# Performance work log

Measured on AMD Instinct MI355X. Metric: run time of the kernel, lower is better.

The kernel has to match this reference:

```python
import jax, jax.numpy as jnp
import numpy as np
from jax import lax

L = 25            # max_delay (250 // init_spike_step=10, odd)
SIG = 12.0        # max_delay // 2, frozen (requires_grad=False)
BN_EPS = 1e-5
EPS = 1e-7


def _dcls_kernel(W, P):
    # Gaussian interpolation of kernel_count=1 weights onto a dense kernel of size L.
    # W, P: (out, in). Returns (out, in, L).
    grid = jnp.arange(L, dtype=W.dtype) - L // 2          # (L,)
    K = jnp.exp(-0.5 * ((grid[None, None, :] - P[:, :, None]) / SIG) ** 2)
    K = K / (jnp.sum(K, axis=-1, keepdims=True) + EPS)    # normalize over kernel taps
    return W[:, :, None] * K


def _dcls_conv(x_tbc, W, P):
    # x_tbc: (T, B, Cin) -> causal dilated-kernel conv over time -> (T, B, Cout)
    kernel = _dcls_kernel(W, P)                           # (Cout, Cin, L)
    xb = jnp.transpose(x_tbc, (1, 2, 0))                  # (B, Cin, T)
    xb = jnp.pad(xb, ((0, 0), (0, 0), (L - 1, 0)))        # left (causal) padding
    y = lax.conv_general_dilated(xb, kernel, window_strides=(1,), padding='VALID',
                                 dimension_numbers=('NCH', 'OIH', 'NCH'))
    return jnp.transpose(y, (2, 0, 1))                    # (T, B, Cout)


def _bn(x_tbc, gamma, beta):
    # BatchNorm1d with step_mode='m': stats over merged (T, B) per channel.
    mean = jnp.mean(x_tbc, axis=(0, 1))
    var = jnp.var(x_tbc, axis=(0, 1))
    xhat = (x_tbc - mean) * lax.rsqrt(var + BN_EPS)
    return gamma * xhat + beta


def setup_inputs() -> dict:
    key = jax.random.key(0)
    ks = jax.random.split(key, 8)
    B, T, C = 128, 100, 700
    x = jax.random.uniform(ks[0], (B, T, C), dtype=jnp.float32)
    pmax = float(L // 2)
    W1 = jax.random.normal(ks[1], (256, 700), jnp.float32) * (1.0 / np.sqrt(700))
    P1 = jax.random.uniform(ks[2], (256, 700), jnp.float32, minval=-pmax, maxval=pmax)
    W2 = jax.random.normal(ks[3], (256, 256), jnp.float32) * (1.0 / np.sqrt(256))
    P2 = jax.random.uniform(ks[4], (256, 256), jnp.float32, minval=-pmax, maxval=pmax)
    W3 = jax.random.normal(ks[5], (20, 256), jnp.float32) * (1.0 / np.sqrt(256))
    P3 = jax.random.uniform(ks[6], (20, 256), jnp.float32, minval=-pmax, maxval=pmax)
    return {
        'x': x, 'W1': W1, 'P1': P1, 'W2': W2, 'P2': P2, 'W3': W3, 'P3': P3,
        'gamma1': jnp.ones((256,), jnp.float32), 'beta1': jnp.zeros((256,), jnp.float32),
        'gamma2': jnp.ones((256,), jnp.float32), 'beta2': jnp.zeros((256,), jnp.float32),
    }


def reference(x, W1, P1, W2, P2, W3, P3, gamma1, beta1, gamma2, beta2):
    h = jnp.transpose(x, (1, 0, 2))            # (T, B, C)
    h = _dcls_conv(h, W1, P1)                  # (T, B, 256)
    h = jax.nn.relu(_bn(h, gamma1, beta1))     # dropout = identity (eval)
    h = _dcls_conv(h, W2, P2)                  # (T, B, 256)
    h = jax.nn.relu(_bn(h, gamma2, beta2))
    h = _dcls_conv(h, W3, P3)                  # (T, B, 20)
    return jnp.sum(jax.nn.softmax(h, axis=2), axis=0)   # (B, 20)
```

## Files before the change

### kernel.cpp

```cpp
#include <hip/hip_runtime.h>
#include <stdint.h>


#define T_LEN 100
#define B_SZ  128
#define M_ROWS 12800
#define R_RANK 4
#define K_FIR 448

typedef __bf16 v8bf __attribute__((ext_vector_type(8)));
typedef float  v4f  __attribute__((ext_vector_type(4)));
typedef unsigned int uint32;
typedef unsigned short ushort_t;

struct PhiT { float v[25][R_RANK]; };
constexpr double cexp_(double x) {
  double s = 1.0, t = 1.0;
  for (int n = 1; n < 30; ++n) { t = t * x / n; s += t; }
  return s;
}
constexpr PhiT make_phi() {
  PhiT P{};
  for (int tau = 0; tau < 25; ++tau) {
    double u = (tau - 12) / 12.0;
    double g = cexp_(-0.5 * u * u);
    double T0 = 1.0, T1 = u;
    P.v[tau][0] = (float)(g * T0);
    P.v[tau][1] = (float)(g * T1);
    for (int r = 2; r < R_RANK; ++r) {
      double T2 = 2.0 * u * T1 - T0;
      P.v[tau][r] = (float)(g * T2);
      T0 = T1; T1 = T2;
    }
  }
  return P;
}
constexpr PhiT PHI = make_phi();

__device__ __forceinline__ void gl_lds16(const void* g, void* l) {
  __builtin_amdgcn_global_load_lds(
      (const __attribute__((address_space(1))) char*)g,
      (__attribute__((address_space(3))) char*)l, 16, 0, 0);
}

__device__ __forceinline__ void build_wr_body(
    const float* __restrict__ W, const float* __restrict__ P,
    __bf16* __restrict__ Wr, int CIN, int CINP, int COUT, int COUTP, int o) {
  for (int i = threadIdx.x; i < CINP; i += blockDim.x) {
    bool valid = (o < COUT) && (i < CIN);
    float w = valid ? W[(size_t)o * CIN + i] : 0.f;
    float p = valid ? P[(size_t)o * CIN + i] : 0.f;
    float S = 0.f;
#pragma unroll
    for (int l = 0; l < 25; ++l) {
      float d = ((float)(l - 12) - p) * (1.f / 12.f);
      S += expf(-0.5f * d * d);
    }
    float v = p * (1.f / 12.f);
    float g = w * expf(-0.5f * v * v) / (S + 1e-7f);
    float h = 0.5f * v, hh = h * h;
    float pw = 1.f;
#pragma unroll
    for (int r = 0; r < R_RANK; ++r) {
      float term = pw, sum = pw;
#pragma unroll
      for (int m = 1; m <= 6; ++m) {
        term *= hh / (float)(m * (m + r));
        sum += term;
      }
      float c = g * ((r == 0) ? 1.f : 2.f) * sum;
      Wr[((size_t)r * COUTP + o) * CINP + i] = (__bf16)c;
      pw *= h / (float)(r + 1);
    }
  }
}

__global__ void setup_all(const float* __restrict__ x,
                          const float* __restrict__ W1, const float* __restrict__ P1,
                          const float* __restrict__ W2, const float* __restrict__ P2,
                          const float* __restrict__ W3, const float* __restrict__ P3,
                          __bf16* __restrict__ Xb, __bf16* __restrict__ Wr1,
                          __bf16* __restrict__ Wr2, __bf16* __restrict__ Wr3,
                          __bf16* __restrict__ Af, float* __restrict__ stats) {
  int blk = blockIdx.x;
  if (blk < 256) { build_wr_body(W1, P1, Wr1, 700, 704, 256, 256, blk); return; }
  blk -= 256;
  if (blk < 256) { build_wr_body(W2, P2, Wr2, 256, 256, 256, 256, blk); return; }
  blk -= 256;
  if (blk < 32) { build_wr_body(W3, P3, Wr3, 256, 256, 20, 32, blk); return; }
  blk -= 32;
  if (blk < 196) {
    int idx = blk * 256 + threadIdx.x;
    if (idx < 112 * 448) {
      int t = idx / 448, k = idx - t * 448;
      float v = 0.f;
      if (t < 100 && k < 400) {
        int r = k / 100, s = k - r * 100;
        int tau = s - t + 24;
        if (tau >= 0 && tau < 25) v = PHI.v[tau][r];
      }
      Af[idx] = (__bf16)v;
    }
    return;
  }
  blk -= 196;
  if (blk < 12800) {
    int t = blk >> 7, b = blk & 127;
    const float* src = x + ((size_t)b * T_LEN + t) * 700;
    __bf16* dst = Xb + (size_t)blk * 704;
    for (int c = threadIdx.x; c < 704; c += 256) dst[c] = (c < 700) ? (__bf16)src[c] : (__bf16)0.f;
    return;
  }
  blk -= 12800;
  if (blk == 0) {
    for (int i = threadIdx.x; i < 1024; i += 256) stats[i] = 0.f;
  }
}

template <int CINP, int BLK_N, int WROWS, int WCOLS, int CO_SH, bool BN>
__global__ __launch_bounds__(256, 2)
void gemm_rk64(const __bf16* __restrict__ A, const __bf16* __restrict__ Bm,
               __bf16* __restrict__ Z,
               const float* __restrict__ stats, const float* __restrict__ gamma,
               const float* __restrict__ beta) {
  constexpr int COUTP = 1 << CO_SH;
  constexpr int WM = 128 / WROWS;
  constexpr int WN = BLK_N / WCOLS;
  constexpr int RM = WM / 16;
  constexpr int RN = WN / 16;
  __shared__ __align__(16) __bf16 sA[128 * 64];
  __shared__ __align__(16) __bf16 sB[BLK_N * 64];
  __shared__ float sScale[BN ? 256 : 1];
  __shared__ float sShift[BN ? 256 : 1];

  const int tid = threadIdx.x;
  const int w = tid >> 6, lane = tid & 63;
  const int q = lane >> 4, ln = lane & 15;
  const int wrow = w / WCOLS, wcol = w % WCOLS;
  const int srow8 = lane >> 3;
  const int s8 = lane & 7;
  const int g_lane = s8 ^ srow8;

  const int t0 = blockIdx.x;
  const int oc = blockIdx.y * BLK_N;
  const __bf16* Abase = A + (size_t)t0 * 128 * CINP;
  const __bf16* Bbase = Bm + (size_t)oc * CINP;

  if (BN) {
    int c = tid;
    float mean = stats[c] * (1.f / 12800.f);
    float var = stats[256 + c] * (1.f / 12800.f) - mean * mean;
    float sc = rsqrtf(var + 1e-5f) * gamma[c];
    sScale[c] = sc;
    sShift[c] = beta[c] - mean * sc;
    __syncthreads();
  }

  v4f acc[RM][RN];
#pragma unroll
  for (int a = 0; a < RM; ++a)
#pragma unroll
    for (int b = 0; b < RN; ++b) acc[a][b] = v4f{0.f, 0.f, 0.f, 0.f};

  for (int ic = 0; ic < CINP; ic += 64) {
    if (!BN) {
      for (int j = w; j < 16; j += 4) {
        int m = j * 8 + srow8;
        int g = s8 ^ (m & 7);
        gl_lds16(Abase + (size_t)m * CINP + ic + g * 8, &sA[j * 512]);
      }
    } else {
      float scl[8], sht[8];
#pragma unroll
      for (int jj = 0; jj < 8; ++jj) {
        scl[jj] = sScale[ic + g_lane * 8 + jj];
        sht[jj] = sShift[ic + g_lane * 8 + jj];
      }
      for (int j = w; j < 16; j += 4) {
        int m = j * 8 + srow8;
        uint4 raw = *(const uint4*)(Abase + (size_t)m * CINP + ic + g_lane * 8);
        const ushort_t* pr = (const ushort_t*)&raw;
        uint4 outv;
        ushort_t* po = (ushort_t*)&outv;
#pragma unroll
        for (int jj = 0; jj < 8; ++jj) {
          uint32 u = (uint32)pr[jj] << 16;
          float yv; __builtin_memcpy(&yv, &u, 4);
          float vv = fmaxf(yv * scl[jj] + sht[jj], 0.f);
          __bf16 bv = (__bf16)vv;
          po[jj] = *(const ushort_t*)&bv;
        }
        *(uint4*)((char*)sA + (size_t)j * 1024 + (size_t)lane * 16) = outv;
      }
    }
    for (int j = w; j < BLK_N / 8; j += 4) {
      int n = j * 8 + srow8;
      int g = s8 ^ (n & 7);
      gl_lds16(Bbase + (size_t)n * CINP + ic + g * 8, &sB[j * 512]);
    }
    __syncthreads();

#pragma unroll
    for (int s = 0; s < 2; ++s) {
      v8bf af[RM], bfr[RN];
#pragma unroll
      for (int a = 0; a < RM; ++a) {
        int m = wrow * WM + a * 16 + ln;
        af[a] = *(const v8bf*)&sA[m * 64 + ((((s << 2) | q) ^ (m & 7)) * 8)];
      }
#pragma unroll
      for (int b = 0; b < RN; ++b) {
        int n = wcol * WN + b * 16 + ln;
        bfr[b] = *(const v8bf*)&sB[n * 64 + ((((s << 2) | q) ^ (n & 7)) * 8)];
      }
#pragma unroll
      for (int a = 0; a < RM; ++a)
#pragma unroll
        for (int b = 0; b < RN; ++b)
          acc[a][b] = __builtin_amdgcn_mfma_f32_16x16x32_bf16(af[a], bfr[b], acc[a][b], 0, 0, 0);
    }
    __syncthreads();
  }

#pragma unroll
  for (int a = 0; a < RM; ++a) {
#pragma unroll
    for (int b = 0; b < RN; ++b) {
      int n = oc + wcol * WN + b * 16 + ln;
      int r = n >> CO_SH, o = n & (COUTP - 1);
#pragma unroll
      for (int rr = 0; rr < 4; ++rr) {
        int m = t0 * 128 + wrow * WM + a * 16 + q * 4 + rr;
        Z[((size_t)r * M_ROWS + m) * COUTP + o] = (__bf16)acc[a][b][rr];
      }
    }
  }
}

template <int COUTP, bool STATS, bool SOFTMAX>
__global__ __launch_bounds__(256, 2)
void fir_gemm64(const __bf16* __restrict__ Af, const __bf16* __restrict__ Z,
                __bf16* __restrict__ Yout, float* __restrict__ stats,
                float* __restrict__ outp, int N) {
  __shared__ __align__(16) unsigned char smem[26624];
  __bf16* sA = (__bf16*)smem;
  uint32* sBu = (uint32*)(smem + 14336);

  const int tid = threadIdx.x;
  const int w = tid >> 6, lane = tid & 63;
  const int q = lane >> 4, ln = lane & 15;
  const int srow8 = lane >> 3, s8 = lane & 7;
  const int kp = tid >> 3;
  const int noct = tid & 7;
  const int nb = blockIdx.x * 64;

  v4f acc[7];
#pragma unroll
  for (int a = 0; a < 7; ++a) acc[a] = v4f{0.f, 0.f, 0.f, 0.f};

  for (int kc = 0; kc < K_FIR; kc += 64) {
    for (int j = w; j < 14; j += 4) {
      int m = j * 8 + srow8;
      int g = s8 ^ (m & 7);
      gl_lds16(Af + (size_t)m * K_FIR + kc + g * 8, &sA[j * 512]);
    }
    const __bf16* zp = Z + (size_t)(kc + kp * 2) * N + nb + noct * 8;
    uint4 r0 = *(const uint4*)zp;
    uint4 r1 = *(const uint4*)(zp + N);
    const ushort_t* p0 = (const ushort_t*)&r0;
    const ushort_t* p1 = (const ushort_t*)&r1;
#pragma unroll
    for (int j = 0; j < 8; ++j) {
      uint32 val = (uint32)p0[j] | ((uint32)p1[j] << 16);
      sBu[(noct * 8 + j) * 35 + kp] = val;
    }
    __syncthreads();

#pragma unroll
    for (int s = 0; s < 2; ++s) {
      v8bf af[7];
#pragma unroll
      for (int a = 0; a < 7; ++a) {
        int m = a * 16 + ln;
        af[a] = *(const v8bf*)&sA[m * 64 + ((((s << 2) | q) ^ (m & 7)) * 8)];
      }
      int base = (w * 16 + ln) * 35 + s * 16 + q * 4;
      uint32 tmp[4] = {sBu[base], sBu[base + 1], sBu[base + 2], sBu[base + 3]};
      v8bf bfr = *(const v8bf*)tmp;
#pragma unroll
      for (int a = 0; a < 7; ++a)
        acc[a] = __builtin_amdgcn_mfma_f32_16x16x32_bf16(af[a], bfr, acc[a], 0, 0, 0);
    }
    __syncthreads();
  }

  int ng = nb + w * 16 + ln;
  if (!SOFTMAX) {
    float s = 0.f, ss = 0.f;
#pragma unroll
    for (int a = 0; a < 7; ++a) {
#pragma unroll
      for (int rr = 0; rr < 4; ++rr) {
        int t = a * 16 + q * 4 + rr;
        float v = acc[a][rr];
        if (t < 100) {
          Yout[(size_t)t * N + ng] = (__bf16)v;
          s += v; ss += v * v;
        }
      }
    }
    if (STATS) {
      s += __shfl_xor(s, 16); ss += __shfl_xor(ss, 16);
      s += __shfl_xor(s, 32); ss += __shfl_xor(ss, 32);
      if (q == 0) {
        int o = ng & (COUTP - 1);
        atomicAdd(&stats[o], s);
        atomicAdd(&stats[COUTP + o], ss);
      }
    }
  } else {
    float* smx = (float*)smem;
    float* lacc = (float*)(smem + 26000);
    int col = w * 16 + ln;
#pragma unroll
    for (int a = 0; a < 7; ++a) {
#pragma unroll
      for (int rr = 0; rr < 4; ++rr) {
        int t = a * 16 + q * 4 + rr;
        if (t < 100) smx[t * 65 + col] = acc[a][rr];
      }
    }
    if (tid < 64) lacc[tid & 63] = 0.f;
    __syncthreads();
    if (tid < 200) {
      int bl = tid / 100, t = tid - bl * 100;
      const float* rr = &smx[t * 65 + bl * 32];
      float v[20], m = -1e30f;
#pragma unroll
      for (int o = 0; o < 20; ++o) { v[o] = rr[o]; m = fmaxf(m, v[o]); }
      float sum = 0.f;
#pragma unroll
      for (int o = 0; o < 20; ++o) { v[o] = expf(v[o] - m); sum += v[o]; }
      float inv = 1.f / sum;
#pragma unroll
      for (int o = 0; o < 20; ++o) atomicAdd(&lacc[bl * 20 + o], v[o] * inv);
    }
    __syncthreads();
    if (tid < 40) {
      int bl = tid / 20, o = tid - bl * 20;
      int b = (nb >> 5) + bl;
      outp[b * 20 + o] = lacc[bl * 20 + o];
    }
  }
}


extern "C" void kernel_launch(void* const* d_in, const int* in_sizes, int n_in,
                              void* d_out, int out_size, void* d_ws, size_t ws_size,
                              hipStream_t stream) {
  const float* x  = (const float*)d_in[0];
  const float* W1 = (const float*)d_in[1];
  const float* P1 = (const float*)d_in[2];
  const float* W2 = (const float*)d_in[3];
  const float* P2 = (const float*)d_in[4];
  const float* W3 = (const float*)d_in[5];
  const float* P3 = (const float*)d_in[6];
  const float* g1 = (const float*)d_in[7];
  const float* b1 = (const float*)d_in[8];
  const float* g2 = (const float*)d_in[9];
  const float* b2 = (const float*)d_in[10];
  float* out = (float*)d_out;

  constexpr size_t XB_B  = (size_t)M_ROWS * 704 * 2;
  constexpr size_t Z_B   = (size_t)K_FIR * 32768 * 2;
  constexpr size_t Y12_B = (size_t)M_ROWS * 256 * 2;
  constexpr size_t W1_B  = (size_t)R_RANK * 256 * 704 * 2;
  constexpr size_t W2_B  = (size_t)R_RANK * 256 * 256 * 2;
  constexpr size_t W3_B  = (size_t)R_RANK * 32 * 256 * 2;
  constexpr size_t AF_B  = (size_t)112 * K_FIR * 2;
  constexpr size_t ST_B  = 4096;
  constexpr size_t TOTAL = XB_B + Z_B + Y12_B + W1_B + W2_B + W3_B + AF_B + ST_B;
  if (ws_size < TOTAL) return;

  char* ws = (char*)d_ws;
  size_t off = 0;
  __bf16* Xb   = (__bf16*)(ws + off); off += XB_B;
  __bf16* Zb   = (__bf16*)(ws + off); off += Z_B;
  __bf16* Yb   = (__bf16*)(ws + off); off += Y12_B;
  __bf16* Wr1  = (__bf16*)(ws + off); off += W1_B;
  __bf16* Wr2  = (__bf16*)(ws + off); off += W2_B;
  __bf16* Wr3  = (__bf16*)(ws + off); off += W3_B;
  __bf16* Afir = (__bf16*)(ws + off); off += AF_B;
  float*  stats1 = (float*)(ws + off);
  float*  stats2 = stats1 + 512;

  setup_all<<<dim3(13541), 256, 0, stream>>>(x, W1, P1, W2, P2, W3, P3,
                                             Xb, Wr1, Wr2, Wr3, Afir, stats1);

  gemm_rk64<704, 128, 2, 2, 8, false><<<dim3(100, 8), 256, 0, stream>>>(
      Xb, Wr1, Zb, nullptr, nullptr, nullptr);
  fir_gemm64<256, true, false><<<dim3(512), 256, 0, stream>>>(
      Afir, Zb, Yb, stats1, nullptr, 32768);

  gemm_rk64<256, 128, 2, 2, 8, true><<<dim3(100, 8), 256, 0, stream>>>(
      Yb, Wr2, Zb, stats1, g1, b1);
  fir_gemm64<256, true, false><<<dim3(512), 256, 0, stream>>>(
      Afir, Zb, Yb, stats2, nullptr, 32768);

  gemm_rk64<256, 64, 2, 2, 5, true><<<dim3(100, 2), 256, 0, stream>>>(
      Yb, Wr3, Zb, stats2, g2, b2);
  fir_gemm64<32, false, true><<<dim3(64), 256, 0, stream>>>(
      Afir, Zb, nullptr, nullptr, out, 4096);
}
```

Before: 209.8 us.

## Unfuse BN+ReLU into standalone kernel and widen GEMM N-tile to 256

Moves the BatchNorm scale/shift and ReLU out of the GEMM A-tile load into a separate elementwise kernel that rewrites the bf16 activations in place. The GEMM can then use async global-to-LDS loads for A, and the first two GEMMs switch to a 256-wide output tile, so each A tile is loaded once instead of twice. The cost is an extra kernel launch plus a full read-write pass over the 12800x256 activations per layer. The larger tile also uses more LDS and accumulator registers per block, which may lower occupancy.

```diff
diff --git a/kernel.cpp b/kernel.cpp
--- a/kernel.cpp
+++ b/kernel.cpp
@@ -117,12 +117,10 @@
   }
 }
 
-template <int CINP, int BLK_N, int WROWS, int WCOLS, int CO_SH, bool BN>
+template <int CINP, int BLK_N, int WROWS, int WCOLS, int CO_SH>
 __global__ __launch_bounds__(256, 2)
 void gemm_rk64(const __bf16* __restrict__ A, const __bf16* __restrict__ Bm,
-               __bf16* __restrict__ Z,
-               const float* __restrict__ stats, const float* __restrict__ gamma,
-               const float* __restrict__ beta) {
+               __bf16* __restrict__ Z) {
   constexpr int COUTP = 1 << CO_SH;
   constexpr int WM = 128 / WROWS;
   constexpr int WN = BLK_N / WCOLS;
@@ -130,8 +128,6 @@
   constexpr int RN = WN / 16;
   __shared__ __align__(16) __bf16 sA[128 * 64];
   __shared__ __align__(16) __bf16 sB[BLK_N * 64];
-  __shared__ float sScale[BN ? 256 : 1];
-  __shared__ float sShift[BN ? 256 : 1];
 
   const int tid = threadIdx.x;
   const int w = tid >> 6, lane = tid & 63;
@@ -139,23 +135,12 @@
   const int wrow = w / WCOLS, wcol = w % WCOLS;
   const int srow8 = lane >> 3;
   const int s8 = lane & 7;
-  const int g_lane = s8 ^ srow8;
 
   const int t0 = blockIdx.x;
   const int oc = blockIdx.y * BLK_N;
   const __bf16* Abase = A + (size_t)t0 * 128 * CINP;
   const __bf16* Bbase = Bm + (size_t)oc * CINP;
 
-  if (BN) {
-    int c = tid;
-    float mean = stats[c] * (1.f / 12800.f);
-    float var = stats[256 + c] * (1.f / 12800.f) - mean * mean;
-    float sc = rsqrtf(var + 1e-5f) * gamma[c];
-    sScale[c] = sc;
-    sShift[c] = beta[c] - mean * sc;
-    __syncthreads();
-  }
-
   v4f acc[RM][RN];
 #pragma unroll
   for (int a = 0; a < RM; ++a)
@@ -163,35 +148,10 @@
     for (int b = 0; b < RN; ++b) acc[a][b] = v4f{0.f, 0.f, 0.f, 0.f};
 
   for (int ic = 0; ic < CINP; ic += 64) {
-    if (!BN) {
-      for (int j = w; j < 16; j += 4) {
-        int m = j * 8 + srow8;
-        int g = s8 ^ (m & 7);
-        gl_lds16(Abase + (size_t)m * CINP + ic + g * 8, &sA[j * 512]);
-      }
-    } else {
-      float scl[8], sht[8];
-#pragma unroll
-      for (int jj = 0; jj < 8; ++jj) {
-        scl[jj] = sScale[ic + g_lane * 8 + jj];
-        sht[jj] = sShift[ic + g_lane * 8 + jj];
-      }
-      for (int j = w; j < 16; j += 4) {
-        int m = j * 8 + srow8;
-        uint4 raw = *(const uint4*)(Abase + (size_t)m * CINP + ic + g_lane * 8);
-        const ushort_t* pr = (const ushort_t*)&raw;
-        uint4 outv;
-        ushort_t* po = (ushort_t*)&outv;
-#pragma unroll
-        for (int jj = 0; jj < 8; ++jj) {
-          uint32 u = (uint32)pr[jj] << 16;
-          float yv; __builtin_memcpy(&yv, &u, 4);
-          float vv = fmaxf(yv * scl[jj] + sht[jj], 0.f);
-          __bf16 bv = (__bf16)vv;
-          po[jj] = *(const ushort_t*)&bv;
-        }
-        *(uint4*)((char*)sA + (size_t)j * 1024 + (size_t)lane * 16) = outv;
-      }
+    for (int j = w; j < 16; j += 4) {
+      int m = j * 8 + srow8;
+      int g = s8 ^ (m & 7);
+      gl_lds16(Abase + (size_t)m * CINP + ic + g * 8, &sA[j * 512]);
     }
     for (int j = w; j < BLK_N / 8; j += 4) {
       int n = j * 8 + srow8;
@@ -352,6 +312,33 @@
       outp[b * 20 + o] = lacc[bl * 20 + o];
     }
   }
+}
+
+__global__ __launch_bounds__(256)
+void bn_apply_relu8(__bf16* __restrict__ h, const float* __restrict__ stats,
+                    const float* __restrict__ gamma, const float* __restrict__ beta) {
+  int idx = blockIdx.x * 256 + threadIdx.x;
+  int co = (idx & 31) * 8;
+  size_t row = (size_t)(idx >> 5);
+  __bf16* p = h + row * 256 + co;
+  uint4 raw = *(const uint4*)p;
+  const ushort_t* pr = (const ushort_t*)&raw;
+  uint4 outv;
+  ushort_t* po = (ushort_t*)&outv;
+#pragma unroll
+  for (int j = 0; j < 8; ++j) {
+    int c = co + j;
+    float mean = stats[c] * (1.f / 12800.f);
+    float var = stats[256 + c] * (1.f / 12800.f) - mean * mean;
+    float inv = rsqrtf(var + 1e-5f) * gamma[c];
+    uint32 u = (uint32)pr[j] << 16;
+    float xv; __builtin_memcpy(&xv, &u, 4);
+    float v = (xv - mean) * inv + beta[c];
+    v = fmaxf(v, 0.f);
+    __bf16 bv = (__bf16)v;
+    po[j] = *(const ushort_t*)&bv;
+  }
+  *(uint4*)p = outv;
 }
 
 
@@ -397,18 +384,17 @@
   setup_all<<<dim3(13541), 256, 0, stream>>>(x, W1, P1, W2, P2, W3, P3,
                                              Xb, Wr1, Wr2, Wr3, Afir, stats1);
 
-  gemm_rk64<704, 128, 2, 2, 8, false><<<dim3(100, 8), 256, 0, stream>>>(
-      Xb, Wr1, Zb, nullptr, nullptr, nullptr);
+  gemm_rk64<704, 256, 2, 2, 8><<<dim3(100, 4), 256, 0, stream>>>(Xb, Wr1, Zb);
   fir_gemm64<256, true, false><<<dim3(512), 256, 0, stream>>>(
       Afir, Zb, Yb, stats1, nullptr, 32768);
-
-  gemm_rk64<256, 128, 2, 2, 8, true><<<dim3(100, 8), 256, 0, stream>>>(
-      Yb, Wr2, Zb, stats1, g1, b1);
+  bn_apply_relu8<<<dim3(1600), 256, 0, stream>>>(Yb, stats1, g1, b1);
+
+  gemm_rk64<256, 256, 2, 2, 8><<<dim3(100, 4), 256, 0, stream>>>(Yb, Wr2, Zb);
   fir_gemm64<256, true, false><<<dim3(512), 256, 0, stream>>>(
       Afir, Zb, Yb, stats2, nullptr, 32768);
-
-  gemm_rk64<256, 64, 2, 2, 5, true><<<dim3(100, 2), 256, 0, stream>>>(
-      Yb, Wr3, Zb, stats2, g2, b2);
+  bn_apply_relu8<<<dim3(1600), 256, 0, stream>>>(Yb, stats2, g2, b2);
+
+  gemm_rk64<256, 64, 2, 2, 5><<<dim3(100, 2), 256, 0, stream>>>(Yb, Wr3, Zb);
   fir_gemm64<32, false, true><<<dim3(64), 256, 0, stream>>>(
       Afir, Zb, nullptr, nullptr, out, 4096);
 }
```

New measurement: 200.5 us, median of 2. -4.4%, faster.
